# Kernel optimization log

Measured on AMD Instinct MI355X. Metric: run time of the kernel, lower is better.

The kernel has to match this reference:

```python
import jax, jax.numpy as jnp
import numpy as np

# BTT factorization dims: d_in = m1*m2 = 4096, d_out = n1*n2 = 4096, rs = (1, R, 1)
B = 4096
M1 = 64
M2 = 64
N1 = 64
N2 = 64
R = 4  # tt_rank


def setup_inputs() -> dict:
    key = jax.random.key(0)
    kx, k1, k2 = jax.random.split(key, 3)
    # xavier_normal_(W, gain=1/sqrt(fan_in_factor)); fan_in/out of xavier use last two dims
    std1 = (1.0 / (M1 * 1) ** 0.5) * (2.0 / (M1 * 1 + N1 * R)) ** 0.5
    std2 = (1.0 / (M2 * R) ** 0.5) * (2.0 / (M2 * R + N2 * 1)) ** 0.5
    x = jax.random.normal(kx, (B, M1 * M2), dtype=jnp.float32)
    W1 = jax.random.normal(k1, (M2, M1 * 1, N1 * R), dtype=jnp.float32) * std1
    W2 = jax.random.normal(k2, (N1, M2 * R, N2 * 1), dtype=jnp.float32) * std2
    return {"x": x, "W1": W1, "W2": W2}


def reference(x, W1, W2):
    b = x.shape[0]
    # stage 1: contract m1, batched over m2 -> intermediate (b, m2, n1, r2)
    xr = x.reshape(b, M2, M1)                             # (b, m2, m1)
    t = jnp.einsum('bma,mac->bmc', xr, W1)                # (b, m2, n1*r2)
    t = t.reshape(b, M2, N1, R)                           # (b, m2, n1, r2)
    # stage 2: contract (m2, r2), batched over n1 -> (b, n1, n2)
    t = t.transpose(0, 2, 1, 3).reshape(b, N1, M2 * R)    # (b, n1, m2*r2)
    y = jnp.einsum('bnd,ndo->bno', t, W2)                 # (b, n1, n2)
    return y.reshape(b, N1 * N2)
```

## Files before the change

kernel.cpp:

```cpp
#include <hip/hip_runtime.h>

typedef unsigned short u16;
typedef unsigned int u32;
typedef __attribute__((ext_vector_type(8))) short short8;
typedef __attribute__((ext_vector_type(4))) float f32x4;

__device__ __forceinline__ u16 f2bf(float f) {
    union { float f; u32 u; } c; c.f = f;
    u32 u = c.u;
    return (u16)((u + 0x7fffu + ((u >> 16) & 1u)) >> 16);
}

#define MFMA16(A, B, C) __builtin_amdgcn_mfma_f32_16x16x32_bf16((A), (B), (C), 0, 0, 0)

__global__ __launch_bounds__(256) void prep_w(const float* __restrict__ W1,
                                              const float* __restrict__ W2,
                                              u16* __restrict__ W1F,
                                              u16* __restrict__ W2F) {
    __shared__ u16 sh[16384];
    const int bid = blockIdx.x;
    const int t = threadIdx.x;

    if (bid < 64) {
        const int m2 = bid;
        const float4* src = (const float4*)(W1 + (size_t)m2 * 16384);
        #pragma unroll
        for (int s = 0; s < 16; ++s) {
            float4 f = src[s * 256 + t];
            float fv[4] = {f.x, f.y, f.z, f.w};
            #pragma unroll
            for (int e = 0; e < 4; ++e) {
                int elem = (s * 256 + t) * 4 + e;
                int m1 = elem >> 8, c = elem & 255;
                int nb = c >> 5, ct = (c >> 4) & 1, lr = c & 15;
                int ks = m1 >> 5, q = (m1 >> 3) & 3, j = m1 & 7;
                sh[(((((nb * 2 + ct) * 2 + ks) * 4 + q)) << 7) + lr * 8 + j] =
                    f2bf(fv[e]);
            }
        }
        __syncthreads();
        u16* dst = W1F + (size_t)m2 * 16384 + t * 64;
        #pragma unroll
        for (int s = 0; s < 8; ++s)
            *(short8*)(dst + s * 8) = *(const short8*)(&sh[t * 64 + s * 8]);
    } else {
        const int n1 = bid - 64;
        const float4* src = (const float4*)(W2 + (size_t)n1 * 16384);
        #pragma unroll
        for (int s = 0; s < 16; ++s) {
            float4 f = src[s * 256 + t];
            float fv[4] = {f.x, f.y, f.z, f.w};
            #pragma unroll
            for (int e = 0; e < 4; ++e) {
                int elem = (s * 256 + t) * 4 + e;
                int k = elem >> 6, n2 = elem & 63;
                int m2b = k >> 5, q = (k >> 3) & 3, j = k & 7;
                int nt = n2 >> 4, lr = n2 & 15;
                sh[((((m2b * 4 + nt) * 4 + q)) << 7) + lr * 8 + j] = f2bf(fv[e]);
            }
        }
        __syncthreads();
        u16* dst = W2F + (size_t)n1 * 16384 + t * 64;
        #pragma unroll
        for (int s = 0; s < 8; ++s)
            *(short8*)(dst + s * 8) = *(const short8*)(&sh[t * 64 + s * 8]);
    }
}

__global__ __launch_bounds__(512) void btt_fused(const float* __restrict__ x,
                                                 const u16* __restrict__ W1F,
                                                 const u16* __restrict__ W2F,
                                                 float* __restrict__ out) {
    __shared__ u16 t_lds[32 * 260];

    const int tid = threadIdx.x;
    const int w = tid >> 6;
    const int lane = tid & 63;
    const int q = lane >> 4;
    const int lr = lane & 15;
    const int bt = blockIdx.x & 127;
    const int nb = blockIdx.x >> 7;
    const int n1 = nb * 8 + w;

    const f32x4 fz = {0.f, 0.f, 0.f, 0.f};
    f32x4 acc2[2][4];
    #pragma unroll
    for (int i = 0; i < 2; ++i)
        #pragma unroll
        for (int j = 0; j < 4; ++j) acc2[i][j] = fz;

    for (int m2b = 0; m2b < 8; ++m2b) {
        const int m2 = m2b * 8 + w;

        short8 a1[2][2];
        {
            const u16* p = W1F + ((size_t)m2 * 8 + nb) * 2048 + lane * 8;
            #pragma unroll
            for (int ct = 0; ct < 2; ++ct)
                #pragma unroll
                for (int ks = 0; ks < 2; ++ks)
                    a1[ct][ks] = *(const short8*)(p + (ct * 2 + ks) * 512);
        }
        short8 b2[4];
        {
            const u16* p = W2F + (size_t)n1 * 16384 + m2b * 2048 + lane * 8;
            #pragma unroll
            for (int nt = 0; nt < 4; ++nt)
                b2[nt] = *(const short8*)(p + nt * 512);
        }
        short8 bx[2][2];
        #pragma unroll
        for (int bl = 0; bl < 2; ++bl)
            #pragma unroll
            for (int ks = 0; ks < 2; ++ks) {
                const float* p = x + (size_t)(bt * 32 + bl * 16 + lr) * 4096 +
                                 m2 * 64 + ks * 32 + q * 8;
                float4 ua = *(const float4*)(p);
                float4 ub = *(const float4*)(p + 4);
                short8 r;
                r[0] = (short)f2bf(ua.x); r[1] = (short)f2bf(ua.y);
                r[2] = (short)f2bf(ua.z); r[3] = (short)f2bf(ua.w);
                r[4] = (short)f2bf(ub.x); r[5] = (short)f2bf(ub.y);
                r[6] = (short)f2bf(ub.z); r[7] = (short)f2bf(ub.w);
                bx[bl][ks] = r;
            }

        f32x4 acc1[2][2];
        #pragma unroll
        for (int ct = 0; ct < 2; ++ct)
            #pragma unroll
            for (int bl = 0; bl < 2; ++bl) acc1[ct][bl] = fz;
        #pragma unroll
        for (int ks = 0; ks < 2; ++ks)
            #pragma unroll
            for (int ct = 0; ct < 2; ++ct)
                #pragma unroll
                for (int bl = 0; bl < 2; ++bl)
                    acc1[ct][bl] = MFMA16(a1[ct][ks], bx[bl][ks], acc1[ct][bl]);

        __syncthreads();

        #pragma unroll
        for (int ct = 0; ct < 2; ++ct)
            #pragma unroll
            for (int bl = 0; bl < 2; ++bl) {
                int off = (bl * 16 + lr) * 260 + w * 32 + ct * 16 + q * 4;
                u32 lo = (u32)f2bf(acc1[ct][bl][0]) | ((u32)f2bf(acc1[ct][bl][1]) << 16);
                u32 hi = (u32)f2bf(acc1[ct][bl][2]) | ((u32)f2bf(acc1[ct][bl][3]) << 16);
                *(uint2*)(&t_lds[off]) = make_uint2(lo, hi);
            }

        __syncthreads();

        short8 a2[2];
        #pragma unroll
        for (int bl = 0; bl < 2; ++bl) {
            int base = (bl * 16 + lr) * 260 + (2 * q) * 32 + w * 4;
            union { short8 v; uint2 u[2]; } tmp;
            tmp.u[0] = *(const uint2*)(&t_lds[base]);
            tmp.u[1] = *(const uint2*)(&t_lds[base + 32]);
            a2[bl] = tmp.v;
        }
        #pragma unroll
        for (int bl = 0; bl < 2; ++bl)
            #pragma unroll
            for (int nt = 0; nt < 4; ++nt)
                acc2[bl][nt] = MFMA16(a2[bl], b2[nt], acc2[bl][nt]);
    }

    #pragma unroll
    for (int bl = 0; bl < 2; ++bl)
        #pragma unroll
        for (int nt = 0; nt < 4; ++nt)
            #pragma unroll
            for (int g = 0; g < 4; ++g) {
                long row = bt * 32 + bl * 16 + q * 4 + g;
                long col = (long)n1 * 64 + nt * 16 + lr;
                out[row * 4096 + col] = acc2[bl][nt][g];
            }
}

__global__ __launch_bounds__(512) void btt_nows(const float* __restrict__ x,
                                                const float* __restrict__ W1,
                                                const float* __restrict__ W2,
                                                float* __restrict__ out) {
    __shared__ u16 t_lds[64 * 260];
    const int tid = threadIdx.x;
    const int w = tid >> 6;
    const int lane = tid & 63;
    const int q = lane >> 4;
    const int lr = lane & 15;
    const int bt = blockIdx.x & 63;
    const int nb = blockIdx.x >> 6;
    const int n1 = nb * 8 + w;

    const f32x4 fz = {0.f, 0.f, 0.f, 0.f};
    f32x4 acc2[4][4];
    #pragma unroll
    for (int i = 0; i < 4; ++i)
        #pragma unroll
        for (int j = 0; j < 4; ++j) acc2[i][j] = fz;

    for (int m2b = 0; m2b < 8; ++m2b) {
        const int m2 = m2b * 8 + w;
        short8 ax[4][2];
        #pragma unroll
        for (int bl = 0; bl < 4; ++bl)
            #pragma unroll
            for (int ks = 0; ks < 2; ++ks) {
                const float* p = x + (size_t)(bt * 64 + bl * 16 + lr) * 4096 +
                                 m2 * 64 + ks * 32 + q * 8;
                float4 ua = *(const float4*)(p);
                float4 ub = *(const float4*)(p + 4);
                short8 r;
                r[0] = (short)f2bf(ua.x); r[1] = (short)f2bf(ua.y);
                r[2] = (short)f2bf(ua.z); r[3] = (short)f2bf(ua.w);
                r[4] = (short)f2bf(ub.x); r[5] = (short)f2bf(ub.y);
                r[6] = (short)f2bf(ub.z); r[7] = (short)f2bf(ub.w);
                ax[bl][ks] = r;
            }
        short8 bw1[2][2];
        #pragma unroll
        for (int ct = 0; ct < 2; ++ct)
            #pragma unroll
            for (int ks = 0; ks < 2; ++ks)
                #pragma unroll
                for (int j = 0; j < 8; ++j)
                    bw1[ct][ks][j] = (short)f2bf(W1[m2 * 16384 +
                                                    (ks * 32 + q * 8 + j) * 256 +
                                                    nb * 32 + ct * 16 + lr]);
        f32x4 acc1[4][2];
        #pragma unroll
        for (int bl = 0; bl < 4; ++bl)
            #pragma unroll
            for (int ct = 0; ct < 2; ++ct) acc1[bl][ct] = fz;
        #pragma unroll
        for (int ks = 0; ks < 2; ++ks)
            #pragma unroll
            for (int bl = 0; bl < 4; ++bl)
                #pragma unroll
                for (int ct = 0; ct < 2; ++ct)
                    acc1[bl][ct] = MFMA16(ax[bl][ks], bw1[ct][ks], acc1[bl][ct]);

        __syncthreads();
        #pragma unroll
        for (int bl = 0; bl < 4; ++bl)
            #pragma unroll
            for (int ct = 0; ct < 2; ++ct)
                #pragma unroll
                for (int g = 0; g < 4; ++g)
                    t_lds[(bl * 16 + q * 4 + g) * 260 + w * 32 + ct * 16 + lr] =
                        f2bf(acc1[bl][ct][g]);
        __syncthreads();

        short8 a2[4];
        #pragma unroll
        for (int bl = 0; bl < 4; ++bl) {
            int base = (bl * 16 + lr) * 260 + (2 * q) * 32 + w * 4;
            union { short8 v; uint2 u[2]; } tmp;
            tmp.u[0] = *(const uint2*)(&t_lds[base]);
            tmp.u[1] = *(const uint2*)(&t_lds[base + 32]);
            a2[bl] = tmp.v;
        }
        short8 b2[4];
        #pragma unroll
        for (int nt = 0; nt < 4; ++nt)
            #pragma unroll
            for (int j = 0; j < 8; ++j)
                b2[nt][j] = (short)f2bf(W2[n1 * 16384 +
                                           (m2b * 32 + q * 8 + j) * 64 +
                                           nt * 16 + lr]);
        #pragma unroll
        for (int bl = 0; bl < 4; ++bl)
            #pragma unroll
            for (int nt = 0; nt < 4; ++nt)
                acc2[bl][nt] = MFMA16(a2[bl], b2[nt], acc2[bl][nt]);
    }

    #pragma unroll
    for (int bl = 0; bl < 4; ++bl)
        #pragma unroll
        for (int nt = 0; nt < 4; ++nt)
            #pragma unroll
            for (int g = 0; g < 4; ++g) {
                long row = bt * 64 + bl * 16 + q * 4 + g;
                long col = (long)n1 * 64 + nt * 16 + lr;
                out[row * 4096 + col] = acc2[bl][nt][g];
            }
}

extern "C" void kernel_launch(void* const* d_in, const int* in_sizes, int n_in,
                              void* d_out, int out_size, void* d_ws, size_t ws_size,
                              hipStream_t stream) {
    const float* x  = (const float*)d_in[0];
    const float* W1 = (const float*)d_in[1];
    const float* W2 = (const float*)d_in[2];
    float* out = (float*)d_out;

    const size_t N_W1F = (size_t)64 * 16384;
    const size_t N_W2F = (size_t)64 * 16384;
    const size_t WS_NEED = (N_W1F + N_W2F) * sizeof(u16);

    if (ws_size >= WS_NEED) {
        u16* W1F = (u16*)d_ws;
        u16* W2F = W1F + N_W1F;
        prep_w<<<128, 256, 0, stream>>>(W1, W2, W1F, W2F);
        btt_fused<<<1024, 512, 0, stream>>>(x, W1F, W2F, out);
    } else {
        btt_nows<<<512, 512, 0, stream>>>(x, W1, W2, out);
    }
}
```

Measured before the change: 191.3 us.

## Double the batch tile to 64 rows and double-buffer the LDS intermediate

```diff
diff --git a/kernel.cpp b/kernel.cpp
--- a/kernel.cpp
+++ b/kernel.cpp
@@ -67,114 +67,114 @@
     }
 }
 
-__global__ __launch_bounds__(512) void btt_fused(const float* __restrict__ x,
-                                                 const u16* __restrict__ W1F,
-                                                 const u16* __restrict__ W2F,
-                                                 float* __restrict__ out) {
-    __shared__ u16 t_lds[32 * 260];
+__global__ __launch_bounds__(512) void btt_f64(const float* __restrict__ x,
+                                               const u16* __restrict__ W1F,
+                                               const u16* __restrict__ W2F,
+                                               float* __restrict__ out) {
+    __shared__ u16 t_lds[2][64 * 260];
 
     const int tid = threadIdx.x;
     const int w = tid >> 6;
     const int lane = tid & 63;
     const int q = lane >> 4;
     const int lr = lane & 15;
-    const int bt = blockIdx.x & 127;
-    const int nb = blockIdx.x >> 7;
+    const int bt = blockIdx.x & 63;
+    const int nb = blockIdx.x >> 6;
     const int n1 = nb * 8 + w;
 
     const f32x4 fz = {0.f, 0.f, 0.f, 0.f};
-    f32x4 acc2[2][4];
+    f32x4 acc2[4][4];
     #pragma unroll
-    for (int i = 0; i < 2; ++i)
+    for (int i = 0; i < 4; ++i)
         #pragma unroll
         for (int j = 0; j < 4; ++j) acc2[i][j] = fz;
 
     for (int m2b = 0; m2b < 8; ++m2b) {
         const int m2 = m2b * 8 + w;
+        const int p = m2b & 1;
 
         short8 a1[2][2];
         {
-            const u16* p = W1F + ((size_t)m2 * 8 + nb) * 2048 + lane * 8;
+            const u16* pw = W1F + ((size_t)m2 * 8 + nb) * 2048 + lane * 8;
             #pragma unroll
             for (int ct = 0; ct < 2; ++ct)
                 #pragma unroll
                 for (int ks = 0; ks < 2; ++ks)
-                    a1[ct][ks] = *(const short8*)(p + (ct * 2 + ks) * 512);
+                    a1[ct][ks] = *(const short8*)(pw + (ct * 2 + ks) * 512);
         }
         short8 b2[4];
         {
-            const u16* p = W2F + (size_t)n1 * 16384 + m2b * 2048 + lane * 8;
+            const u16* pw = W2F + (size_t)n1 * 16384 + m2b * 2048 + lane * 8;
             #pragma unroll
             for (int nt = 0; nt < 4; ++nt)
-                b2[nt] = *(const short8*)(p + nt * 512);
-        }
-        short8 bx[2][2];
-        #pragma unroll
-        for (int bl = 0; bl < 2; ++bl)
+                b2[nt] = *(const short8*)(pw + nt * 512);
+        }
+
+        short8 ax[4][2];
+        #pragma unroll
+        for (int bl = 0; bl < 4; ++bl)
             #pragma unroll
             for (int ks = 0; ks < 2; ++ks) {
-                const float* p = x + (size_t)(bt * 32 + bl * 16 + lr) * 4096 +
-                                 m2 * 64 + ks * 32 + q * 8;
-                float4 ua = *(const float4*)(p);
-                float4 ub = *(const float4*)(p + 4);
+                const float* px = x + (size_t)(bt * 64 + bl * 16 + lr) * 4096 +
+                                  m2 * 64 + ks * 32 + q * 8;
+                float4 ua = *(const float4*)(px);
+                float4 ub = *(const float4*)(px + 4);
                 short8 r;
                 r[0] = (short)f2bf(ua.x); r[1] = (short)f2bf(ua.y);
                 r[2] = (short)f2bf(ua.z); r[3] = (short)f2bf(ua.w);
                 r[4] = (short)f2bf(ub.x); r[5] = (short)f2bf(ub.y);
                 r[6] = (short)f2bf(ub.z); r[7] = (short)f2bf(ub.w);
-                bx[bl][ks] = r;
-            }
-
-        f32x4 acc1[2][2];
+                ax[bl][ks] = r;
+            }
+
+        f32x4 acc1[2][4];
         #pragma unroll
         for (int ct = 0; ct < 2; ++ct)
             #pragma unroll
-            for (int bl = 0; bl < 2; ++bl) acc1[ct][bl] = fz;
+            for (int bl = 0; bl < 4; ++bl) acc1[ct][bl] = fz;
         #pragma unroll
         for (int ks = 0; ks < 2; ++ks)
             #pragma unroll
             for (int ct = 0; ct < 2; ++ct)
                 #pragma unroll
-                for (int bl = 0; bl < 2; ++bl)
-                    acc1[ct][bl] = MFMA16(a1[ct][ks], bx[bl][ks], acc1[ct][bl]);
-
-        __syncthreads();
+                for (int bl = 0; bl < 4; ++bl)
+                    acc1[ct][bl] = MFMA16(a1[ct][ks], ax[bl][ks], acc1[ct][bl]);
 
         #pragma unroll
         for (int ct = 0; ct < 2; ++ct)
             #pragma unroll
-            for (int bl = 0; bl < 2; ++bl) {
+            for (int bl = 0; bl < 4; ++bl) {
                 int off = (bl * 16 + lr) * 260 + w * 32 + ct * 16 + q * 4;
                 u32 lo = (u32)f2bf(acc1[ct][bl][0]) | ((u32)f2bf(acc1[ct][bl][1]) << 16);
                 u32 hi = (u32)f2bf(acc1[ct][bl][2]) | ((u32)f2bf(acc1[ct][bl][3]) << 16);
-                *(uint2*)(&t_lds[off]) = make_uint2(lo, hi);
-            }
-
-        __syncthreads();
-
-        short8 a2[2];
-        #pragma unroll
-        for (int bl = 0; bl < 2; ++bl) {
+                *(uint2*)(&t_lds[p][off]) = make_uint2(lo, hi);
+            }
+
+        __syncthreads();
+
+        short8 a2[4];
+        #pragma unroll
+        for (int bl = 0; bl < 4; ++bl) {
             int base = (bl * 16 + lr) * 260 + (2 * q) * 32 + w * 4;
             union { short8 v; uint2 u[2]; } tmp;
-            tmp.u[0] = *(const uint2*)(&t_lds[base]);
-            tmp.u[1] = *(const uint2*)(&t_lds[base + 32]);
+            tmp.u[0] = *(const uint2*)(&t_lds[p][base]);
+            tmp.u[1] = *(const uint2*)(&t_lds[p][base + 32]);
             a2[bl] = tmp.v;
         }
         #pragma unroll
-        for (int bl = 0; bl < 2; ++bl)
+        for (int bl = 0; bl < 4; ++bl)
             #pragma unroll
             for (int nt = 0; nt < 4; ++nt)
                 acc2[bl][nt] = MFMA16(a2[bl], b2[nt], acc2[bl][nt]);
     }
 
     #pragma unroll
-    for (int bl = 0; bl < 2; ++bl)
+    for (int bl = 0; bl < 4; ++bl)
         #pragma unroll
         for (int nt = 0; nt < 4; ++nt)
             #pragma unroll
             for (int g = 0; g < 4; ++g) {
-                long row = bt * 32 + bl * 16 + q * 4 + g;
+                long row = bt * 64 + bl * 16 + q * 4 + g;
                 long col = (long)n1 * 64 + nt * 16 + lr;
                 out[row * 4096 + col] = acc2[bl][nt][g];
             }
@@ -305,7 +305,7 @@
         u16* W1F = (u16*)d_ws;
         u16* W2F = W1F + N_W1F;
         prep_w<<<128, 256, 0, stream>>>(W1, W2, W1F, W2F);
-        btt_fused<<<1024, 512, 0, stream>>>(x, W1F, W2F, out);
+        btt_f64<<<512, 512, 0, stream>>>(x, W1F, W2F, out);
     } else {
         btt_nows<<<512, 512, 0, stream>>>(x, W1, W2, out);
     }
```

New measurement: 199.2 us. 4.1% more time.
